# Performance work log

Measured on AMD Instinct MI355X. Metric: run time of the kernel, lower is better.

Reference implementation:

```python
import jax, jax.numpy as jnp
import numpy as np

D_MODEL = 2048
NUM_HEADS = 16
D_K = D_MODEL // NUM_HEADS  # 128
THETA = 10000.0
B, S = 4, 2048


def _apply_rope(t, token_positions, theta=THETA):
    # t: [B, H, S, d_k]; rotate interleaved (even, odd) pairs
    d_k = t.shape[-1]
    inv_freq = 1.0 / (theta ** (jnp.arange(0, d_k, 2, dtype=jnp.float32) / d_k))  # [d_k/2]
    angles = token_positions.astype(jnp.float32)[:, None] * inv_freq[None, :]     # [S, d_k/2]
    cos = jnp.cos(angles)  # [S, d_k/2]
    sin = jnp.sin(angles)
    t1 = t[..., 0::2]  # [B,H,S,d_k/2]
    t2 = t[..., 1::2]
    r1 = t1 * cos - t2 * sin
    r2 = t1 * sin + t2 * cos
    out = jnp.stack([r1, r2], axis=-1)  # [B,H,S,d_k/2,2]
    return out.reshape(t.shape)


def setup_inputs() -> dict:
    key = jax.random.key(0)
    ks = jax.random.split(key, 5)
    scale = 0.02
    return {
        "x": jax.random.normal(ks[0], (B, S, D_MODEL), dtype=jnp.float32),
        "token_positions": jnp.arange(S, dtype=jnp.int64 if jax.config.jax_enable_x64 else jnp.int32),
        "Wq": jax.random.normal(ks[1], (D_MODEL, D_MODEL), dtype=jnp.float32) * scale,
        "Wk": jax.random.normal(ks[2], (D_MODEL, D_MODEL), dtype=jnp.float32) * scale,
        "Wv": jax.random.normal(ks[3], (D_MODEL, D_MODEL), dtype=jnp.float32) * scale,
        "Wo": jax.random.normal(ks[4], (D_MODEL, D_MODEL), dtype=jnp.float32) * scale,
    }


def reference(x, token_positions, Wq, Wk, Wv, Wo):
    # Linear(in, out): weight [out, in], y = x @ W.T (no bias)
    q = jnp.einsum('bsd,ed->bse', x, Wq)
    k = jnp.einsum('bsd,ed->bse', x, Wk)
    v = jnp.einsum('bsd,ed->bse', x, Wv)
    # split heads: [B, S, H*dk] -> [B, H, S, dk]
    def split(t):
        return t.reshape(B, S, NUM_HEADS, D_K).transpose(0, 2, 1, 3)
    qh, kh, vh = split(q), split(k), split(v)
    qh = _apply_rope(qh, token_positions)
    kh = _apply_rope(kh, token_positions)
    scores = jnp.einsum('bhqd,bhkd->bhqk', qh, kh) / jnp.sqrt(jnp.float32(D_K))
    causal = jnp.tril(jnp.ones((S, S), dtype=bool))
    scores = jnp.where(causal[None, None], scores, jnp.finfo(scores.dtype).min)
    attn = jax.nn.softmax(scores, axis=-1)
    attended = jnp.einsum('bhqk,bhkd->bhqd', attn, vh)  # [B,H,S,dk]
    merged = attended.transpose(0, 2, 1, 3).reshape(B, S, D_MODEL)
    return jnp.einsum('bsd,ed->bse', merged, Wo)
```

## Files before the change

### kernel.cpp

```cpp
#include <hip/hip_runtime.h>
#include <stdint.h>


using u16 = unsigned short;
typedef __bf16 bf16_t;
typedef __bf16 bf16x8 __attribute__((ext_vector_type(8)));
typedef float  f32x4  __attribute__((ext_vector_type(4)));
typedef u16    u16x4  __attribute__((ext_vector_type(4)));

#define DEVI static __device__ __forceinline__
#define AS1 __attribute__((address_space(1)))
#define AS3 __attribute__((address_space(3)))
#define GLL16(g,l) __builtin_amdgcn_global_load_lds((const AS1 void*)(g), (AS3 void*)(l), 16, 0, 0)

DEVI u16 f2bf(float x){ bf16_t h=(bf16_t)x; return __builtin_bit_cast(u16,h); }
DEVI f32x4 mfma16(bf16x8 a, bf16x8 b, f32x4 c){
  return __builtin_amdgcn_mfma_f32_16x16x32_bf16(a,b,c,0,0,0);
}

__global__ __launch_bounds__(256) void k_cvt(const float* __restrict__ in, u16* __restrict__ out){
  int i = blockIdx.x*256 + threadIdx.x;
  float4 v = ((const float4*)in)[i];
  u16x4 o = { f2bf(v.x), f2bf(v.y), f2bf(v.z), f2bf(v.w) };
  ((u16x4*)out)[i] = o;
}

__global__ __launch_bounds__(256) void k_tab(const int* __restrict__ pos, float* __restrict__ ct, float* __restrict__ stab){
  int i = blockIdx.x*256 + threadIdx.x;
  int s = i>>6, f = i&63;
  float inv = __expf(-0.14391275442161033f * (float)f);
  float a = (float)pos[s] * inv;
  float sv, cv; sincosf(a, &sv, &cv);
  ct[i] = cv; stab[i] = sv;
}

template<int EPI>
__global__ __launch_bounds__(512,2) void k_gemm(
    const bf16_t* __restrict__ A, const bf16_t* __restrict__ Bt,
    void* __restrict__ O0, void* __restrict__ O1, void* __restrict__ O2,
    const float* __restrict__ ct, const float* __restrict__ stab)
{
  __shared__ char Al[2][32768];
  __shared__ char Bl[2][32768];
  const int tid = threadIdx.x, wave = tid>>6, lane = tid&63;
  const int rgrp = lane>>4, cidx = lane&15;
  const int wm = wave>>2, wn = wave&3;
  constexpr int NB = (EPI==4)? 24 : 8;
  const int bid = blockIdx.x;
  const int wg = (bid&7)*(4*NB) + (bid>>3);
  const int by = wg & 31, bx = wg >> 5;
  const int bm = by*256, bn = bx*256;

  const char* Ag = (const char*)A  + (size_t)bm*4096;
  const char* Bg = (const char*)Bt + (size_t)bn*4096;

  const int swz  = (cidx&7)<<4;
  const int sgsw = ((lane&7)*16) ^ ((lane>>3)<<4);
  const int arow0 = wm*128 + wn*32 + (lane>>3);
  const int brow0 = (wn>>1)*128 + (wm*2+(wn&1))*32 + (lane>>3);
  const int adst0 = (wm*128 + wn*32)*128;
  const int bdst0 = ((wn>>1)*128 + (wm*2+(wn&1))*32)*128;

  f32x4 acc[2][4][4] = {};
  bf16x8 af[4], bfA[4], bfB[4];

#define STAGE_A(b, kt2) do{ _Pragma("unroll") \
  for (int g=0; g<4; ++g) \
    GLL16(Ag + (size_t)(arow0 + g*8)*4096 + (kt2)*128 + sgsw, &Al[b][adst0 + g*1024]); }while(0)
#define STAGE_B(b, kt2) do{ _Pragma("unroll") \
  for (int g=0; g<4; ++g) \
    GLL16(Bg + (size_t)(brow0 + g*8)*4096 + (kt2)*128 + sgsw, &Bl[b][bdst0 + g*1024]); }while(0)
#define LOAD_AF(MH, KK) do{ _Pragma("unroll") \
  for (int fi=0; fi<4; ++fi) \
    af[fi] = *(const bf16x8*)&Al[cur][(((wm*128 + (MH)*64 + fi*16 + cidx)*128 + (KK)*64 + rgrp*16) ^ swz)]; }while(0)
#define LOAD_BF(DST, KK) do{ _Pragma("unroll") \
  for (int fj=0; fj<4; ++fj) \
    DST[fj] = *(const bf16x8*)&Bl[cur][(((wn*64 + fj*16 + cidx)*128 + (KK)*64 + rgrp*16) ^ swz)]; }while(0)
#define PHASE_TAIL(MH, BFR) do{ \
  __builtin_amdgcn_s_barrier(); \
  asm volatile("s_waitcnt lgkmcnt(0)" ::: "memory"); \
  __builtin_amdgcn_sched_barrier(0); \
  __builtin_amdgcn_s_setprio(1); \
  _Pragma("unroll") for (int fi=0; fi<4; ++fi){ \
    _Pragma("unroll") for (int fj=0; fj<4; ++fj){ \
      acc[MH][fi][fj] = mfma16(af[fi], BFR[fj], acc[MH][fi][fj]); }} \
  __builtin_amdgcn_s_setprio(0); \
  __builtin_amdgcn_sched_barrier(0); \
  __builtin_amdgcn_s_barrier(); }while(0)

  STAGE_A(0, 0); STAGE_B(0, 0);
  asm volatile("s_waitcnt vmcnt(0)" ::: "memory");
  __builtin_amdgcn_s_barrier();
  int cur = 0;
  for (int t=0; t<32; ++t){
    const bool pf = (t < 31);
    if (pf) STAGE_A(cur^1, t+1);
    LOAD_AF(0,0); LOAD_BF(bfA, 0);
    PHASE_TAIL(0, bfA);
    if (pf) STAGE_B(cur^1, t+1);
    LOAD_AF(1,0);
    PHASE_TAIL(1, bfA);
    LOAD_AF(0,1); LOAD_BF(bfB, 1);
    PHASE_TAIL(0, bfB);
    LOAD_AF(1,1);
    PHASE_TAIL(1, bfB);
    asm volatile("s_waitcnt vmcnt(0)" ::: "memory");
    __builtin_amdgcn_s_barrier();
    __builtin_amdgcn_sched_barrier(0);
    cur ^= 1;
  }
#undef STAGE_A
#undef STAGE_B
#undef LOAD_AF
#undef LOAD_BF
#undef PHASE_TAIL

  if constexpr (EPI==3){
    float* O = (float*)O0;
    #pragma unroll
    for (int mh=0; mh<2; ++mh)
      #pragma unroll
      for (int fi=0; fi<4; ++fi){
        const int m0 = bm + wm*128 + mh*64 + fi*16 + rgrp*4;
        #pragma unroll
        for (int fj=0; fj<4; ++fj){
          const int n = bn + wn*64 + fj*16 + cidx;
          #pragma unroll
          for (int r=0; r<4; ++r)
            O[(size_t)(m0+r)*2048 + n] = acc[mh][fi][fj][r];
        }
      }
  } else {
    const int seg = bn>>11;
    if (seg==2){
      u16* O = (u16*)O2;
      #pragma unroll
      for (int mh=0; mh<2; ++mh)
        #pragma unroll
        for (int fi=0; fi<4; ++fi){
          const int m0 = bm + wm*128 + mh*64 + fi*16 + rgrp*4;
          const int b = m0>>11, s0 = m0&2047;
          #pragma unroll
          for (int fj=0; fj<4; ++fj){
            const int nl = (bn + wn*64 + fj*16 + cidx) & 2047;
            const int h = nl>>7, d = nl&127;
            u16x4 pk = { f2bf(acc[mh][fi][fj][0]), f2bf(acc[mh][fi][fj][1]),
                         f2bf(acc[mh][fi][fj][2]), f2bf(acc[mh][fi][fj][3]) };
            *(u16x4*)(O + ((size_t)((b*16+h)*128 + d)*2048 + s0)) = pk;
          }
        }
    } else {
      u16* O = seg ? (u16*)O1 : (u16*)O0;
      const float qs = seg ? 1.0f : 0.08838834764831845f;
      #pragma unroll
      for (int fj=0; fj<4; ++fj){
        const int nl = (bn + wn*64 + fj*16 + cidx) & 2047;
        const int h = nl>>7, d = nl&127, f = (nl&127)>>1;
        #pragma unroll
        for (int mh=0; mh<2; ++mh)
          #pragma unroll
          for (int fi=0; fi<4; ++fi){
            #pragma unroll
            for (int r=0; r<4; ++r){
              const int m = bm + wm*128 + mh*64 + fi*16 + rgrp*4 + r;
              const int b = m>>11, s = m&2047;
              float v = acc[mh][fi][fj][r];
              float p = __shfl_xor(v, 1, 64);
              float cv = ct[s*64+f], sv = stab[s*64+f];
              float o = (d&1) ? (p*sv + v*cv) : (v*cv - p*sv);
              o *= qs;
              O[(size_t)(b*16+h)*262144 + (size_t)s*128 + d] = f2bf(o);
            }
          }
      }
    }
  }
}

__global__ __launch_bounds__(256,2) void k_attn(
  const bf16_t* __restrict__ Q, const bf16_t* __restrict__ K,
  const bf16_t* __restrict__ Vt, u16* __restrict__ Mg)
{
  __shared__ char kl[2][16384];
  __shared__ char vl[2][16384];
  __shared__ char pl[4][4096];
  const int tid=threadIdx.x, wave=tid>>6, lane=tid&63;
  const int rgrp=lane>>4, cidx=lane&15;
  const int bid=blockIdx.x;
  const int qt = 15 - (bid>>6);
  const int bh = bid & 63;
  const int qbase = qt*128;
  const int last = 2*qt + 1;

  bf16x8 qf[2][4];
  #pragma unroll
  for (int m=0;m<2;++m){
    const bf16_t* qp = Q + ((size_t)bh*2048 + qbase + wave*32 + m*16 + cidx)*128 + rgrp*8;
    #pragma unroll
    for (int ds=0; ds<4; ++ds) qf[m][ds] = *(const bf16x8*)(qp + ds*32);
  }
  f32x4 oacc[2][8] = {};
  float mrow[2] = {-1e30f,-1e30f};
  float lrow[2] = {0.f,0.f};

  const char* Kg = (const char*)K  + (size_t)bh*524288;
  const char* Vg = (const char*)Vt + (size_t)bh*524288;
  char* pw = pl[wave];
  const int L0 = tid*16;
  const int qrow0 = qbase + wave*32 + cidx;

  #define STAGE(buf, kt_) do{                                                  \
    _Pragma("unroll")                                                          \
    for (int i_=0;i_<4;++i_){                                                  \
      int L_ = i_*4096 + L0;                                                   \
      int row_ = L_>>8;                                                        \
      int in_ = (L_&255) ^ ((row_&7)<<4);                                      \
      GLL16(Kg + (size_t)((kt_)*64+row_)*256 + in_, &kl[buf][i_*4096 + wave*1024]); \
    }                                                                          \
    _Pragma("unroll")                                                          \
    for (int i_=0;i_<4;++i_){                                                  \
      int L_ = i_*4096 + L0;                                                   \
      int d_ = L_>>7;                                                          \
      int in_ = (L_&127) ^ ((d_&7)<<4);                                        \
      GLL16(Vg + (size_t)d_*4096 + (kt_)*128 + in_, &vl[buf][i_*4096 + wave*1024]); \
    }                                                                          \
  }while(0)

  STAGE(0, 0);
  int cur = 0;
  for (int kt=0; kt<=last; ++kt){
    const bool pf = (kt < last);
    if (pf) STAGE(cur^1, kt+1);
    if (pf) asm volatile("s_waitcnt vmcnt(8)" ::: "memory");
    else    asm volatile("s_waitcnt vmcnt(0)" ::: "memory");
    __builtin_amdgcn_s_barrier();

    f32x4 stt[2][4];
    #pragma unroll
    for (int m=0;m<2;++m)
      #pragma unroll
      for (int t=0;t<4;++t) stt[m][t] = (f32x4){0.f,0.f,0.f,0.f};
    __builtin_amdgcn_s_setprio(1);
    #pragma unroll
    for (int t=0;t<4;++t){
      const int krow = t*16 + cidx;
      #pragma unroll
      for (int ds=0; ds<4; ++ds){
        const int off = (krow*256 + ds*64 + rgrp*16) ^ ((krow&7)<<4);
        bf16x8 kf = *(const bf16x8*)(&kl[cur][off]);
        stt[0][t] = mfma16(kf, qf[0][ds], stt[0][t]);
        stt[1][t] = mfma16(kf, qf[1][ds], stt[1][t]);
      }
    }
    __builtin_amdgcn_s_setprio(0);

    if (kt >= 2*qt){
      #pragma unroll
      for (int m=0;m<2;++m){
        const int q = qrow0 + m*16;
        #pragma unroll
        for (int t=0;t<4;++t){
          #pragma unroll
          for (int r=0;r<4;++r){
            const int key = kt*64 + t*16 + rgrp*4 + r;
            if (key > q) stt[m][t][r] = -1e30f;
          }
        }
      }
    }

    #pragma unroll
    for (int m=0;m<2;++m){
      float vm = stt[m][0][0];
      #pragma unroll
      for (int t=0;t<4;++t)
        #pragma unroll
        for (int r=0;r<4;++r) vm = fmaxf(vm, stt[m][t][r]);
      vm = fmaxf(vm, __shfl_xor(vm, 16, 64));
      vm = fmaxf(vm, __shfl_xor(vm, 32, 64));
      if (!__all(vm <= mrow[m] + 8.f)){
        float mn = fmaxf(mrow[m], vm);
        float c = __expf(mrow[m]-mn);
        mrow[m]=mn; lrow[m]*=c;
        float cr0 = __shfl(c, rgrp*4+0, 64), cr1 = __shfl(c, rgrp*4+1, 64);
        float cr2 = __shfl(c, rgrp*4+2, 64), cr3 = __shfl(c, rgrp*4+3, 64);
        #pragma unroll
        for (int d=0;d<8;++d){
          oacc[m][d][0]*=cr0; oacc[m][d][1]*=cr1;
          oacc[m][d][2]*=cr2; oacc[m][d][3]*=cr3;
        }
      }
      float lt = 0.f;
      #pragma unroll
      for (int t=0;t<4;++t)
        #pragma unroll
        for (int r=0;r<4;++r){
          float p = __expf(stt[m][t][r]-mrow[m]);
          stt[m][t][r]=p; lt+=p;
        }
      lt += __shfl_xor(lt, 16, 64);
      lt += __shfl_xor(lt, 32, 64);
      lrow[m] += lt;
    }

    #pragma unroll
    for (int m=0;m<2;++m){
      const int prow = m*16 + cidx;
      char* base = pw + prow*128;
      const int swz = (prow&7)<<4;
      #pragma unroll
      for (int t=0;t<4;++t){
        u16x4 pk = { f2bf(stt[m][t][0]), f2bf(stt[m][t][1]), f2bf(stt[m][t][2]), f2bf(stt[m][t][3]) };
        *(u16x4*)(base + ((t*32 + rgrp*8) ^ swz)) = pk;
      }
    }
    asm volatile("s_waitcnt lgkmcnt(0)" ::: "memory");
    __builtin_amdgcn_sched_barrier(0);

    __builtin_amdgcn_s_setprio(1);
    #pragma unroll
    for (int ks=0; ks<2; ++ks){
      const int swzc = (cidx&7)<<4;
      bf16x8 pa0 = *(const bf16x8*)(pw + (     cidx)*128 + ((ks*64 + rgrp*16) ^ swzc));
      bf16x8 pa1 = *(const bf16x8*)(pw + (16 + cidx)*128 + ((ks*64 + rgrp*16) ^ swzc));
      #pragma unroll
      for (int dsub=0; dsub<8; ++dsub){
        const int d = dsub*16 + cidx;
        const int off = (d*128 + ks*64 + rgrp*16) ^ ((d&7)<<4);
        bf16x8 vf = *(const bf16x8*)(&vl[cur][off]);
        oacc[0][dsub] = mfma16(pa0, vf, oacc[0][dsub]);
        oacc[1][dsub] = mfma16(pa1, vf, oacc[1][dsub]);
      }
    }
    __builtin_amdgcn_s_setprio(0);
    __builtin_amdgcn_s_barrier();
    cur ^= 1;
  }
  #undef STAGE

  const int b = bh>>4, h = bh&15;
  #pragma unroll
  for (int m=0;m<2;++m){
    float linv = 1.f/lrow[m];
    float ir[4];
    #pragma unroll
    for (int r=0;r<4;++r) ir[r] = __shfl(linv, rgrp*4+r, 64);
    #pragma unroll
    for (int dsub=0;dsub<8;++dsub){
      const int col = h*128 + dsub*16 + cidx;
      #pragma unroll
      for (int r=0;r<4;++r){
        const int srow = qbase + wave*32 + m*16 + rgrp*4 + r;
        Mg[((size_t)b*2048 + srow)*2048 + col] = f2bf(oacc[m][dsub][r]*ir[r]);
      }
    }
  }
}

extern "C" void kernel_launch(void* const* d_in, const int* in_sizes, int n_in,
                              void* d_out, int out_size, void* d_ws, size_t ws_size,
                              hipStream_t stream)
{
  (void)in_sizes; (void)n_in; (void)out_size; (void)ws_size;
  const float* x  = (const float*)d_in[0];
  const int*   tp = (const int*)d_in[1];
  const float* Wq = (const float*)d_in[2];
  const float* Wk = (const float*)d_in[3];
  const float* Wv = (const float*)d_in[4];
  const float* Wo = (const float*)d_in[5];

  char* ws = (char*)d_ws;
  bf16_t* xb  = (bf16_t*)(ws);
  bf16_t* wqb = (bf16_t*)(ws + 33554432);
  bf16_t* wkb = (bf16_t*)(ws + 41943040);
  bf16_t* wvb = (bf16_t*)(ws + 50331648);
  bf16_t* wob = (bf16_t*)(ws + 58720256);
  bf16_t* vt  = (bf16_t*)(ws + 67108864);
  float*  ct  = (float*) (ws + 100663296);
  float*  stb = (float*) (ws + 101187584);
  bf16_t* qr  = (bf16_t*)d_out;
  bf16_t* kr  = (bf16_t*)((char*)d_out + 33554432);
  bf16_t* mg  = xb;

  k_cvt<<<16384,256,0,stream>>>(x,  (u16*)xb);
  k_cvt<<< 4096,256,0,stream>>>(Wq, (u16*)wqb);
  k_cvt<<< 4096,256,0,stream>>>(Wk, (u16*)wkb);
  k_cvt<<< 4096,256,0,stream>>>(Wv, (u16*)wvb);
  k_cvt<<< 4096,256,0,stream>>>(Wo, (u16*)wob);
  k_tab<<<  512,256,0,stream>>>(tp, ct, stb);

  k_gemm<4><<<768,512,0,stream>>>(xb, wqb, qr, kr, vt, ct, stb);
  k_attn<<<1024,256,0,stream>>>(qr, kr, vt, (u16*)mg);
  k_gemm<3><<<256,512,0,stream>>>(mg, wob, d_out, nullptr, nullptr, nullptr, nullptr);
}
```

Before: 480.0 us.

## Split GEMM tile staging into quarter loads with finer vmcnt-based pipelining

Restructures the GEMM main loop so A and B tiles are staged in halves or k-slices interleaved across the four MFMA phases, and waits with vmcnt(4) instead of a full vmcnt(0) plus barrier at the end of each iteration. The B LDS buffer is split by k-half with a new swizzle, and the workgroup-to-tile mapping is changed to group rows per XCD. The intent is to overlap global-to-LDS loads with compute and drop a synchronisation point. The finer vmcnt accounting risks reading LDS data before it has landed if the counts are wrong.

Result: slower. 535.9 us (+11.6%).

```diff
diff --git a/kernel.cpp b/kernel.cpp
--- a/kernel.cpp
+++ b/kernel.cpp
@@ -41,42 +41,45 @@
     const float* __restrict__ ct, const float* __restrict__ stab)
 {
   __shared__ char Al[2][32768];
-  __shared__ char Bl[2][32768];
+  __shared__ char Bl[2][2][16384];
   const int tid = threadIdx.x, wave = tid>>6, lane = tid&63;
   const int rgrp = lane>>4, cidx = lane&15;
   const int wm = wave>>2, wn = wave&3;
-  constexpr int NB = (EPI==4)? 24 : 8;
-  const int bid = blockIdx.x;
-  const int wg = (bid&7)*(4*NB) + (bid>>3);
-  const int by = wg & 31, bx = wg >> 5;
+  const int xcd = blockIdx.x & 7, ii = blockIdx.x >> 3;
+  const int by = xcd*4 + (ii&3), bx = ii>>2;
   const int bm = by*256, bn = bx*256;
 
   const char* Ag = (const char*)A  + (size_t)bm*4096;
   const char* Bg = (const char*)Bt + (size_t)bn*4096;
 
-  const int swz  = (cidx&7)<<4;
-  const int sgsw = ((lane&7)*16) ^ ((lane>>3)<<4);
-  const int arow0 = wm*128 + wn*32 + (lane>>3);
-  const int brow0 = (wn>>1)*128 + (wm*2+(wn&1))*32 + (lane>>3);
-  const int adst0 = (wm*128 + wn*32)*128;
-  const int bdst0 = ((wn>>1)*128 + (wm*2+(wn&1))*32)*128;
+  const int ar = lane>>3, ao = (lane&7)*16;
+  const int asrc = ao ^ (ar<<4);
+  const int br = lane>>2, bo = (lane&3)*16;
+  const int bsrc = bo ^ ((br&6)<<3);
+  const int arsw = (cidx&7)<<4;
+  const int brsw = (cidx&6)<<3;
 
   f32x4 acc[2][4][4] = {};
   bf16x8 af[4], bfA[4], bfB[4];
 
-#define STAGE_A(b, kt2) do{ _Pragma("unroll") \
-  for (int g=0; g<4; ++g) \
-    GLL16(Ag + (size_t)(arow0 + g*8)*4096 + (kt2)*128 + sgsw, &Al[b][adst0 + g*1024]); }while(0)
-#define STAGE_B(b, kt2) do{ _Pragma("unroll") \
-  for (int g=0; g<4; ++g) \
-    GLL16(Bg + (size_t)(brow0 + g*8)*4096 + (kt2)*128 + sgsw, &Bl[b][bdst0 + g*1024]); }while(0)
+#define STAGE_AH(b, kt2, h) do{ _Pragma("unroll") \
+  for (int c_=0; c_<2; ++c_){ const int r0_ = c_*128 + (h)*64; \
+    GLL16(Ag + (size_t)(r0_ + wave*8 + ar)*4096 + (size_t)(kt2)*128 + asrc, \
+          &Al[b][(r0_ + wave*8)*128]); } }while(0)
+#define STAGE_BK(b, kt2, kk) do{ _Pragma("unroll") \
+  for (int c_=0; c_<2; ++c_){ const int r0_ = c_*128; \
+    GLL16(Bg + (size_t)(r0_ + wave*16 + br)*4096 + (size_t)(kt2)*128 + (kk)*64 + bsrc, \
+          &Bl[b][kk][(r0_ + wave*16)*64]); } }while(0)
 #define LOAD_AF(MH, KK) do{ _Pragma("unroll") \
   for (int fi=0; fi<4; ++fi) \
-    af[fi] = *(const bf16x8*)&Al[cur][(((wm*128 + (MH)*64 + fi*16 + cidx)*128 + (KK)*64 + rgrp*16) ^ swz)]; }while(0)
+    af[fi] = *(const bf16x8*)&Al[cur][(wm*128 + (MH)*64 + fi*16 + cidx)*128 \
+                                      + (((KK)*64 + rgrp*16) ^ arsw)]; }while(0)
 #define LOAD_BF(DST, KK) do{ _Pragma("unroll") \
   for (int fj=0; fj<4; ++fj) \
-    DST[fj] = *(const bf16x8*)&Bl[cur][(((wn*64 + fj*16 + cidx)*128 + (KK)*64 + rgrp*16) ^ swz)]; }while(0)
+    DST[fj] = *(const bf16x8*)&Bl[cur][KK][(wn*64 + fj*16 + cidx)*64 \
+                                      + ((rgrp*16) ^ brsw)]; }while(0)
 #define PHASE_TAIL(MH, BFR) do{ \
+  asm volatile("s_waitcnt vmcnt(4)" ::: "memory"); \
   __builtin_amdgcn_s_barrier(); \
   asm volatile("s_waitcnt lgkmcnt(0)" ::: "memory"); \
   __builtin_amdgcn_sched_barrier(0); \
@@ -85,32 +88,30 @@
     _Pragma("unroll") for (int fj=0; fj<4; ++fj){ \
       acc[MH][fi][fj] = mfma16(af[fi], BFR[fj], acc[MH][fi][fj]); }} \
   __builtin_amdgcn_s_setprio(0); \
-  __builtin_amdgcn_sched_barrier(0); \
   __builtin_amdgcn_s_barrier(); }while(0)
 
-  STAGE_A(0, 0); STAGE_B(0, 0);
-  asm volatile("s_waitcnt vmcnt(0)" ::: "memory");
+  STAGE_AH(0, 0, 0); STAGE_BK(0, 0, 0); STAGE_AH(0, 0, 1); STAGE_BK(0, 0, 1);
+  asm volatile("s_waitcnt vmcnt(4)" ::: "memory");
   __builtin_amdgcn_s_barrier();
   int cur = 0;
   for (int t=0; t<32; ++t){
     const bool pf = (t < 31);
-    if (pf) STAGE_A(cur^1, t+1);
+    if (pf) STAGE_AH(cur^1, t+1, 0);
     LOAD_AF(0,0); LOAD_BF(bfA, 0);
     PHASE_TAIL(0, bfA);
-    if (pf) STAGE_B(cur^1, t+1);
+    if (pf) STAGE_BK(cur^1, t+1, 0);
     LOAD_AF(1,0);
     PHASE_TAIL(1, bfA);
+    if (pf) STAGE_AH(cur^1, t+1, 1);
     LOAD_AF(0,1); LOAD_BF(bfB, 1);
     PHASE_TAIL(0, bfB);
+    if (pf) STAGE_BK(cur^1, t+1, 1);
     LOAD_AF(1,1);
     PHASE_TAIL(1, bfB);
-    asm volatile("s_waitcnt vmcnt(0)" ::: "memory");
-    __builtin_amdgcn_s_barrier();
-    __builtin_amdgcn_sched_barrier(0);
     cur ^= 1;
   }
-#undef STAGE_A
-#undef STAGE_B
+#undef STAGE_AH
+#undef STAGE_BK
 #undef LOAD_AF
 #undef LOAD_BF
 #undef PHASE_TAIL
```
